# Kernel optimization log

Measured on AMD Instinct MI355X. Metric: run time of the kernel, lower is better.

The kernel has to match this reference:

```python
import jax, jax.numpy as jnp
import numpy as np

ENC_HID = 512
DEC_HID = 1024
ATTN_DIM = 1024
ATTN_IN = ENC_HID * 2 + DEC_HID  # 2048
B, S = 32, 1024


def setup_inputs() -> dict:
    key = jax.random.key(0)
    k1, k2, k3, k4, k5 = jax.random.split(key, 5)
    decoder_hidden = jax.random.normal(k1, (B, DEC_HID), dtype=jnp.float32)
    encoder_outputs = jax.random.normal(k2, (B, S, 2 * ENC_HID), dtype=jnp.float32)
    # nn.Linear(attn_in, attn_dim): weight [attn_dim, attn_in], bias [attn_dim]
    lim = 1.0 / np.sqrt(ATTN_IN)
    W = jax.random.uniform(k3, (ATTN_IN, ATTN_DIM), jnp.float32, -lim, lim)
    b = jax.random.uniform(k4, (ATTN_DIM,), jnp.float32, -lim, lim)
    v = jax.random.uniform(k5, (ATTN_DIM,), jnp.float32, 0.0, 1.0)
    return {"decoder_hidden": decoder_hidden, "encoder_outputs": encoder_outputs,
            "W": W, "b": b, "v": v}


def reference(decoder_hidden, encoder_outputs, W, b, v):
    # Avoid materializing the repeat+concat: split the Linear weight into the
    # decoder-hidden block and the encoder-outputs block. Same math as
    # tanh(Linear(cat([dec_rep, enc], -1))).
    W_dec = W[:DEC_HID]          # [dec_hid, attn_dim]
    W_enc = W[DEC_HID:]          # [2*enc_hid, attn_dim]
    dec_proj = decoder_hidden @ W_dec + b                     # [B, A]
    enc_proj = jnp.einsum('bse,ea->bsa', encoder_outputs, W_enc)  # [B, S, A]
    energy = jnp.tanh(enc_proj + dec_proj[:, None, :])        # [B, S, A]
    attention = jnp.einsum('bsa,a->bs', energy, v)            # [B, S]
    return jax.nn.softmax(attention, axis=1)
```

## Files before the change

### kernel.cpp

```cpp
#include <hip/hip_runtime.h>
#include <stdint.h>

#define ENC2 1024
#define DECH 1024
#define ADIM 1024
#define BB   32
#define SS   1024

typedef _Float16 half_t;
typedef __attribute__((ext_vector_type(8))) _Float16 half8;
typedef __attribute__((ext_vector_type(4))) float    f32x4;

__device__ __forceinline__ void dma16(const half_t* g, half_t* l) {
    __builtin_amdgcn_global_load_lds((const __attribute__((address_space(1))) void*)g,
                                     (__attribute__((address_space(3))) void*)l,
                                     16, 0, 0);
}

__global__ __launch_bounds__(256) void k_wt(const float* __restrict__ W,
                                            half_t* __restrict__ Wt2) {
    __shared__ float tile[32][257];
    const int nb = blockIdx.x >> 5;
    const int ks = blockIdx.x & 31;
    const int t = threadIdx.x;
    #pragma unroll
    for (int i = 0; i < 32; i++) {
        int idx = t + i * 256;
        int kr = idx >> 8, n = idx & 255;
        tile[kr][n] = W[(size_t)(DECH + ks * 32 + kr) * ADIM + nb * 256 + n];
    }
    __syncthreads();
    half_t* reg = Wt2 + ((size_t)(nb * 32 + ks) << 13);
    #pragma unroll
    for (int i = 0; i < 4; i++) {
        int cid = t + i * 256;
        int r = cid >> 2, pos = cid & 3;
        int c = pos ^ ((r >> 1) & 3);
        half8 h;
        #pragma unroll
        for (int e = 0; e < 8; e++) h[e] = (half_t)tile[c * 8 + e][r];
        *(half8*)(reg + r * 32 + pos * 8) = h;
    }
}

__global__ __launch_bounds__(256) void k_dp1(const float* __restrict__ dh,
                                             const float* __restrict__ W,
                                             float* __restrict__ part) {
    __shared__ float red[4][BB][64];
    const int t = threadIdx.x;
    const int ct = blockIdx.x & 15;
    const int kc = blockIdx.x >> 4;
    const int col = ct * 64 + (t & 63);
    const int w = t >> 6;
    const int k0 = kc * 128 + w * 32;
    float wreg[32];
    #pragma unroll
    for (int kk = 0; kk < 32; kk++)
        wreg[kk] = W[(size_t)(k0 + kk) * ADIM + col];
    float s[BB];
    #pragma unroll
    for (int b = 0; b < BB; b++) s[b] = 0.f;
    #pragma unroll
    for (int kk = 0; kk < 32; kk++) {
        #pragma unroll
        for (int b = 0; b < BB; b++)
            s[b] += dh[b * DECH + k0 + kk] * wreg[kk];
    }
    #pragma unroll
    for (int b = 0; b < BB; b++) red[w][b][t & 63] = s[b];
    __syncthreads();
    if (t < 64) {
        for (int b = 0; b < BB; b++)
            part[((size_t)kc * BB + b) * ADIM + ct * 64 + t] =
                red[0][b][t] + red[1][b][t] + red[2][b][t] + red[3][b][t];
    }
}

__global__ __launch_bounds__(256) void k_dp2(const float* __restrict__ part,
                                             const float* __restrict__ bias,
                                             float* __restrict__ decp) {
    const int i = blockIdx.x * 256 + threadIdx.x;
    float s = bias[i & (ADIM - 1)];
    #pragma unroll
    for (int kc = 0; kc < 8; kc++)
        s += part[(size_t)kc * BB * ADIM + i];
    decp[i] = s;
}

#define BM 128
#define BN 256
#define BK 32
#define LDA 40

__global__ __launch_bounds__(512, 4) void k_main(const float* __restrict__ enc,
                                                 const half_t* __restrict__ Wt2,
                                                 const float* __restrict__ decp,
                                                 const float* __restrict__ v,
                                                 float* __restrict__ scores_part) {
    __shared__ half_t lsA[2][BM][LDA];
    __shared__ half_t lsB[2][BN * BK];

    const int bid = blockIdx.x;
    const int mi = (bid >> 5) * 8 + (bid & 7);
    const int nb = (bid >> 3) & 3;
    const int m0 = mi * BM;
    const int t = threadIdx.x;
    const int w = t >> 6, L = t & 63;
    const int wm = w & 1, wn = w >> 1;
    const int lane15 = L & 15, quad = L >> 4;

    const int arow = t & 127;
    const int akc  = (t >> 7) * 8;
    const float* Aptr = enc + (size_t)(m0 + arow) * ENC2 + akc;

    const half_t* Bbase = Wt2 + ((size_t)(nb * 32) << 13);

    f32x4 acc[4][4];
    #pragma unroll
    for (int i = 0; i < 4; i++)
        #pragma unroll
        for (int j = 0; j < 4; j++) acc[i][j] = (f32x4)0.f;

    float4 ra0, ra1;
    auto loadA = [&](int ks) {
        const float* p = Aptr + ks * BK;
        ra0 = *(const float4*)p;
        ra1 = *(const float4*)(p + 4);
    };
    auto writeA = [&](int pb) {
        half8 ha;
        ha[0] = (half_t)ra0.x; ha[1] = (half_t)ra0.y;
        ha[2] = (half_t)ra0.z; ha[3] = (half_t)ra0.w;
        ha[4] = (half_t)ra1.x; ha[5] = (half_t)ra1.y;
        ha[6] = (half_t)ra1.z; ha[7] = (half_t)ra1.w;
        *(half8*)&lsA[pb][arow][akc] = ha;
    };
    auto dmaB = [&](int ks, int pb) {
        #pragma unroll
        for (int jj = 0; jj < 2; jj++) {
            int j = 2 * w + jj;
            dma16(Bbase + ((size_t)ks << 13) + j * 512 + L * 8,
                  &lsB[pb][j * 512]);
        }
    };

    dmaB(0, 0);
    loadA(0);
    writeA(0);
    loadA(1);
    __syncthreads();

    for (int ks = 0; ks < ENC2 / BK; ks++) {
        const int cur = ks & 1;
        if (ks < ENC2 / BK - 1) {
            dmaB(ks + 1, cur ^ 1);
            writeA(cur ^ 1);
            if (ks < ENC2 / BK - 2) loadA(ks + 2);
        }
        half8 af[4], bf[4];
        #pragma unroll
        for (int sm = 0; sm < 4; sm++)
            af[sm] = *(const half8*)&lsA[cur][wm * 64 + sm * 16 + lane15][quad * 8];
        #pragma unroll
        for (int sn = 0; sn < 4; sn++) {
            int r = wn * 64 + sn * 16 + lane15;
            int pos = quad ^ ((r >> 1) & 3);
            bf[sn] = *(const half8*)&lsB[cur][r * 32 + pos * 8];
        }
        #pragma unroll
        for (int sm = 0; sm < 4; sm++)
            #pragma unroll
            for (int sn = 0; sn < 4; sn++)
                acc[sm][sn] = __builtin_amdgcn_mfma_f32_16x16x32_f16(
                    af[sm], bf[sn], acc[sm][sn], 0, 0, 0);
        __syncthreads();
    }

    const int batch = mi >> 3;
    float vv[4], dp[4];
    #pragma unroll
    for (int sn = 0; sn < 4; sn++) {
        int ng = nb * BN + wn * 64 + sn * 16 + lane15;
        vv[sn] = v[ng];
        dp[sn] = decp[(size_t)batch * ADIM + ng];
    }

    float* redL = (float*)&lsA[0][0][0];
    #pragma unroll
    for (int sm = 0; sm < 4; sm++) {
        #pragma unroll
        for (int rr = 0; rr < 4; rr++) {
            float s = 0.f;
            #pragma unroll
            for (int sn = 0; sn < 4; sn++) {
                float x = acc[sm][sn][rr] + dp[sn];
                float e  = __builtin_amdgcn_exp2f(x * 2.8853900817779268f);
                float th = 1.f - 2.f * __builtin_amdgcn_rcpf(e + 1.f);
                s += th * vv[sn];
            }
            s += __shfl_xor(s, 1, 64);
            s += __shfl_xor(s, 2, 64);
            s += __shfl_xor(s, 4, 64);
            s += __shfl_xor(s, 8, 64);
            if (lane15 == 0) {
                int mlocal = wm * 64 + sm * 16 + quad * 4 + rr;
                redL[wn * 128 + mlocal] = s;
            }
        }
    }
    __syncthreads();
    if (t < 128) {
        float s = redL[t] + redL[128 + t] + redL[256 + t] + redL[384 + t];
        scores_part[((size_t)nb << 15) + m0 + t] = s;
    }
}

__global__ __launch_bounds__(256) void k_softmax(const float* __restrict__ sp,
                                                 float* __restrict__ out) {
    __shared__ float red[8];
    const int b = blockIdx.x, t = threadIdx.x;
    float x[4];
    #pragma unroll
    for (int i = 0; i < 4; i++) {
        size_t idx = (size_t)b * SS + t + i * 256;
        x[i] = sp[idx] + sp[(1u << 15) + idx] + sp[(2u << 15) + idx] +
               sp[(3u << 15) + idx];
    }
    float mx = fmaxf(fmaxf(x[0], x[1]), fmaxf(x[2], x[3]));
    #pragma unroll
    for (int d = 1; d < 64; d <<= 1) mx = fmaxf(mx, __shfl_xor(mx, d, 64));
    if ((t & 63) == 0) red[t >> 6] = mx;
    __syncthreads();
    mx = fmaxf(fmaxf(red[0], red[1]), fmaxf(red[2], red[3]));
    float e[4], s = 0.f;
    #pragma unroll
    for (int i = 0; i < 4; i++) {
        e[i] = __builtin_amdgcn_exp2f((x[i] - mx) * 1.4426950408889634f);
        s += e[i];
    }
    #pragma unroll
    for (int d = 1; d < 64; d <<= 1) s += __shfl_xor(s, d, 64);
    if ((t & 63) == 0) red[4 + (t >> 6)] = s;
    __syncthreads();
    s = red[4] + red[5] + red[6] + red[7];
    float inv = 1.f / s;
    #pragma unroll
    for (int i = 0; i < 4; i++) out[(size_t)b * SS + t + i * 256] = e[i] * inv;
}

extern "C" void kernel_launch(void* const* d_in, const int* in_sizes, int n_in,
                              void* d_out, int out_size, void* d_ws, size_t ws_size,
                              hipStream_t stream) {
    const float* dh   = (const float*)d_in[0];
    const float* enc  = (const float*)d_in[1];
    const float* W    = (const float*)d_in[2];
    const float* bias = (const float*)d_in[3];
    const float* v    = (const float*)d_in[4];
    float* out = (float*)d_out;

    char* ws = (char*)d_ws;
    half_t* Wt2   = (half_t*)ws;
    float*  decp  = (float*)(ws + 2u * 1024 * 1024);
    float*  spart = (float*)(ws + 2u * 1024 * 1024 + 128 * 1024);
    float*  dpart = (float*)(ws + 2u * 1024 * 1024 + 640 * 1024);

    k_wt     <<<128, 256, 0, stream>>>(W, Wt2);
    k_dp1    <<<128, 256, 0, stream>>>(dh, W, dpart);
    k_dp2    <<<128, 256, 0, stream>>>(dpart, bias, decp);
    k_main   <<<1024, 512, 0, stream>>>(enc, Wt2, decp, v, spart);
    k_softmax<<<32, 256, 0, stream>>>(spart, out);
}
```

Before: 308.1 us.

## Pre-convert encoder outputs to fp16 tiles and DMA them directly into LDS

Adds a prep pass that converts the fp32 encoder outputs to fp16 in a layout that matches the MFMA tiles. The same launch also fuses the weight transpose and the decoder-projection partial kernels into one grid. The main GEMM then loads A with global_load_lds DMA instead of register loads plus conversion, and folds the dp2 reduction into its epilogue. The cost is an extra 64MB fp16 round trip through the workspace, plus a fallback path that keeps the old code when the workspace is too small.

```diff
diff --git a/kernel.cpp b/kernel.cpp
--- a/kernel.cpp
+++ b/kernel.cpp
@@ -8,6 +8,7 @@
 #define SS   1024
 
 typedef _Float16 half_t;
+typedef __attribute__((ext_vector_type(4))) _Float16 half4;
 typedef __attribute__((ext_vector_type(8))) _Float16 half8;
 typedef __attribute__((ext_vector_type(4))) float    f32x4;
 
@@ -17,12 +18,13 @@
                                      16, 0, 0);
 }
 
-__global__ __launch_bounds__(256) void k_wt(const float* __restrict__ W,
-                                            half_t* __restrict__ Wt2) {
-    __shared__ float tile[32][257];
-    const int nb = blockIdx.x >> 5;
-    const int ks = blockIdx.x & 31;
-    const int t = threadIdx.x;
+
+__device__ __forceinline__ void wt_body(int blk, int t, char* smem,
+                                        const float* __restrict__ W,
+                                        half_t* __restrict__ Wt2) {
+    float (*tile)[257] = (float (*)[257])smem;
+    const int nb = blk >> 5;
+    const int ks = blk & 31;
     #pragma unroll
     for (int i = 0; i < 32; i++) {
         int idx = t + i * 256;
@@ -43,13 +45,13 @@
     }
 }
 
-__global__ __launch_bounds__(256) void k_dp1(const float* __restrict__ dh,
-                                             const float* __restrict__ W,
-                                             float* __restrict__ part) {
-    __shared__ float red[4][BB][64];
-    const int t = threadIdx.x;
-    const int ct = blockIdx.x & 15;
-    const int kc = blockIdx.x >> 4;
+__device__ __forceinline__ void dp1_body(int blk, int t, char* smem,
+                                         const float* __restrict__ dh,
+                                         const float* __restrict__ W,
+                                         float* __restrict__ part) {
+    float (*red)[BB][64] = (float (*)[BB][64])smem;
+    const int ct = blk & 15;
+    const int kc = blk >> 4;
     const int col = ct * 64 + (t & 63);
     const int w = t >> 6;
     const int k0 = kc * 128 + w * 32;
@@ -76,15 +78,47 @@
     }
 }
 
-__global__ __launch_bounds__(256) void k_dp2(const float* __restrict__ part,
-                                             const float* __restrict__ bias,
-                                             float* __restrict__ decp) {
-    const int i = blockIdx.x * 256 + threadIdx.x;
-    float s = bias[i & (ADIM - 1)];
-    #pragma unroll
-    for (int kc = 0; kc < 8; kc++)
-        s += part[(size_t)kc * BB * ADIM + i];
-    decp[i] = s;
+__device__ __forceinline__ void enc16_body(int blk, int t, char* smem,
+                                           const float* __restrict__ enc,
+                                           half_t* __restrict__ e16) {
+    half_t (*Lt)[264] = (half_t (*)[264])smem;
+    const int rblk = blk >> 2, cblk = blk & 3;
+    const int r0 = rblk * 64, k0 = cblk * 256;
+    #pragma unroll
+    for (int i = 0; i < 16; i++) {
+        int row = i * 4 + (t >> 6);
+        int col = (t & 63) * 4;
+        float4 vv = *(const float4*)&enc[(size_t)(r0 + row) * ENC2 + k0 + col];
+        half4 h;
+        h[0] = (half_t)vv.x; h[1] = (half_t)vv.y;
+        h[2] = (half_t)vv.z; h[3] = (half_t)vv.w;
+        *(half4*)&Lt[row][col] = h;
+    }
+    __syncthreads();
+    const int mi = rblk >> 1, p = rblk & 1;
+    const int ks0 = cblk * 8;
+    #pragma unroll
+    for (int j = 0; j < 8; j++) {
+        int u = j * 256 + t;
+        int pair = u >> 6, l = u & 63;
+        int ksl = pair >> 2, quad = pair & 3;
+        half8 h = *(const half8*)&Lt[l][ksl * 32 + quad * 8];
+        size_t chunk = (size_t)(mi * 32 + ks0 + ksl) * 8 + quad * 2 + p;
+        *(half8*)&e16[(chunk << 9) + l * 8] = h;
+    }
+}
+
+__global__ __launch_bounds__(256) void k_prep(const float* __restrict__ enc,
+                                              const float* __restrict__ W,
+                                              const float* __restrict__ dh,
+                                              half_t* __restrict__ e16,
+                                              half_t* __restrict__ Wt2,
+                                              float* __restrict__ dpart) {
+    __shared__ __align__(16) char smem[33792];
+    const int bid = blockIdx.x;
+    if (bid < 2048)       enc16_body(bid, threadIdx.x, smem, enc, e16);
+    else if (bid < 2176)  wt_body(bid - 2048, threadIdx.x, smem, W, Wt2);
+    else                  dp1_body(bid - 2176, threadIdx.x, smem, dh, W, dpart);
 }
 
 #define BM 128
@@ -92,13 +126,14 @@
 #define BK 32
 #define LDA 40
 
-__global__ __launch_bounds__(512, 4) void k_main(const float* __restrict__ enc,
+__global__ __launch_bounds__(512, 4) void k_main(const half_t* __restrict__ encA,
                                                  const half_t* __restrict__ Wt2,
-                                                 const float* __restrict__ decp,
+                                                 const float* __restrict__ dpart,
+                                                 const float* __restrict__ bias,
                                                  const float* __restrict__ v,
                                                  float* __restrict__ scores_part) {
-    __shared__ half_t lsA[2][BM][LDA];
-    __shared__ half_t lsB[2][BN * BK];
+    __shared__ half_t lsA[2][4096];
+    __shared__ half_t lsB[2][8192];
 
     const int bid = blockIdx.x;
     const int mi = (bid >> 5) * 8 + (bid & 7);
@@ -109,10 +144,7 @@
     const int wm = w & 1, wn = w >> 1;
     const int lane15 = L & 15, quad = L >> 4;
 
-    const int arow = t & 127;
-    const int akc  = (t >> 7) * 8;
-    const float* Aptr = enc + (size_t)(m0 + arow) * ENC2 + akc;
-
+    const half_t* Abase = encA + ((size_t)mi << 17);
     const half_t* Bbase = Wt2 + ((size_t)(nb * 32) << 13);
 
     f32x4 acc[4][4];
@@ -121,19 +153,8 @@
         #pragma unroll
         for (int j = 0; j < 4; j++) acc[i][j] = (f32x4)0.f;
 
-    float4 ra0, ra1;
-    auto loadA = [&](int ks) {
-        const float* p = Aptr + ks * BK;
-        ra0 = *(const float4*)p;
-        ra1 = *(const float4*)(p + 4);
-    };
-    auto writeA = [&](int pb) {
-        half8 ha;
-        ha[0] = (half_t)ra0.x; ha[1] = (half_t)ra0.y;
-        ha[2] = (half_t)ra0.z; ha[3] = (half_t)ra0.w;
-        ha[4] = (half_t)ra1.x; ha[5] = (half_t)ra1.y;
-        ha[6] = (half_t)ra1.z; ha[7] = (half_t)ra1.w;
-        *(half8*)&lsA[pb][arow][akc] = ha;
+    auto dmaA = [&](int ks, int pb) {
+        dma16(Abase + (((size_t)ks * 8 + w) << 9) + L * 8, &lsA[pb][w * 512]);
     };
     auto dmaB = [&](int ks, int pb) {
         #pragma unroll
@@ -144,23 +165,21 @@
         }
     };
 
+    dmaA(0, 0);
     dmaB(0, 0);
-    loadA(0);
-    writeA(0);
-    loadA(1);
     __syncthreads();
 
     for (int ks = 0; ks < ENC2 / BK; ks++) {
         const int cur = ks & 1;
         if (ks < ENC2 / BK - 1) {
+            dmaA(ks + 1, cur ^ 1);
             dmaB(ks + 1, cur ^ 1);
-            writeA(cur ^ 1);
-            if (ks < ENC2 / BK - 2) loadA(ks + 2);
         }
         half8 af[4], bf[4];
         #pragma unroll
         for (int sm = 0; sm < 4; sm++)
-            af[sm] = *(const half8*)&lsA[cur][wm * 64 + sm * 16 + lane15][quad * 8];
+            af[sm] = *(const half8*)&lsA[cur][quad * 1024 +
+                                              (wm * 64 + sm * 16 + lane15) * 8];
         #pragma unroll
         for (int sn = 0; sn < 4; sn++) {
             int r = wn * 64 + sn * 16 + lane15;
@@ -182,10 +201,14 @@
     for (int sn = 0; sn < 4; sn++) {
         int ng = nb * BN + wn * 64 + sn * 16 + lane15;
         vv[sn] = v[ng];
-        dp[sn] = decp[(size_t)batch * ADIM + ng];
-    }
-
-    float* redL = (float*)&lsA[0][0][0];
+        float s = bias[ng];
+        #pragma unroll
+        for (int kc = 0; kc < 8; kc++)
+            s += dpart[((size_t)kc * BB + batch) * ADIM + ng];
+        dp[sn] = s;
+    }
+
+    float* redL = (float*)&lsA[0][0];
     #pragma unroll
     for (int sm = 0; sm < 4; sm++) {
         #pragma unroll
@@ -248,6 +271,152 @@
     for (int i = 0; i < 4; i++) out[(size_t)b * SS + t + i * 256] = e[i] * inv;
 }
 
+__global__ __launch_bounds__(256) void k_wt_f(const float* __restrict__ W,
+                                              half_t* __restrict__ Wt2) {
+    __shared__ __align__(16) char smem[32896];
+    wt_body(blockIdx.x, threadIdx.x, smem, W, Wt2);
+}
+
+__global__ __launch_bounds__(256) void k_dp1_f(const float* __restrict__ dh,
+                                               const float* __restrict__ W,
+                                               float* __restrict__ part) {
+    __shared__ __align__(16) char smem[32768];
+    dp1_body(blockIdx.x, threadIdx.x, smem, dh, W, part);
+}
+
+__global__ __launch_bounds__(256) void k_dp2_f(const float* __restrict__ part,
+                                               const float* __restrict__ bias,
+                                               float* __restrict__ decp) {
+    const int i = blockIdx.x * 256 + threadIdx.x;
+    float s = bias[i & (ADIM - 1)];
+    #pragma unroll
+    for (int kc = 0; kc < 8; kc++)
+        s += part[(size_t)kc * BB * ADIM + i];
+    decp[i] = s;
+}
+
+__global__ __launch_bounds__(512, 4) void k_main_reg(const float* __restrict__ enc,
+                                                     const half_t* __restrict__ Wt2,
+                                                     const float* __restrict__ decp,
+                                                     const float* __restrict__ v,
+                                                     float* __restrict__ scores_part) {
+    __shared__ half_t lsA[2][BM][LDA];
+    __shared__ half_t lsB[2][BN * BK];
+
+    const int bid = blockIdx.x;
+    const int mi = (bid >> 5) * 8 + (bid & 7);
+    const int nb = (bid >> 3) & 3;
+    const int m0 = mi * BM;
+    const int t = threadIdx.x;
+    const int w = t >> 6, L = t & 63;
+    const int wm = w & 1, wn = w >> 1;
+    const int lane15 = L & 15, quad = L >> 4;
+
+    const int arow = t & 127;
+    const int akc  = (t >> 7) * 8;
+    const float* Aptr = enc + (size_t)(m0 + arow) * ENC2 + akc;
+    const half_t* Bbase = Wt2 + ((size_t)(nb * 32) << 13);
+
+    f32x4 acc[4][4];
+    #pragma unroll
+    for (int i = 0; i < 4; i++)
+        #pragma unroll
+        for (int j = 0; j < 4; j++) acc[i][j] = (f32x4)0.f;
+
+    float4 ra0, ra1;
+    auto loadA = [&](int ks) {
+        const float* p = Aptr + ks * BK;
+        ra0 = *(const float4*)p;
+        ra1 = *(const float4*)(p + 4);
+    };
+    auto writeA = [&](int pb) {
+        half8 ha;
+        ha[0] = (half_t)ra0.x; ha[1] = (half_t)ra0.y;
+        ha[2] = (half_t)ra0.z; ha[3] = (half_t)ra0.w;
+        ha[4] = (half_t)ra1.x; ha[5] = (half_t)ra1.y;
+        ha[6] = (half_t)ra1.z; ha[7] = (half_t)ra1.w;
+        *(half8*)&lsA[pb][arow][akc] = ha;
+    };
+    auto dmaB = [&](int ks, int pb) {
+        #pragma unroll
+        for (int jj = 0; jj < 2; jj++) {
+            int j = 2 * w + jj;
+            dma16(Bbase + ((size_t)ks << 13) + j * 512 + L * 8,
+                  &lsB[pb][j * 512]);
+        }
+    };
+
+    dmaB(0, 0);
+    loadA(0);
+    writeA(0);
+    loadA(1);
+    __syncthreads();
+
+    for (int ks = 0; ks < ENC2 / BK; ks++) {
+        const int cur = ks & 1;
+        if (ks < ENC2 / BK - 1) {
+            dmaB(ks + 1, cur ^ 1);
+            writeA(cur ^ 1);
+            if (ks < ENC2 / BK - 2) loadA(ks + 2);
+        }
+        half8 af[4], bf[4];
+        #pragma unroll
+        for (int sm = 0; sm < 4; sm++)
+            af[sm] = *(const half8*)&lsA[cur][wm * 64 + sm * 16 + lane15][quad * 8];
+        #pragma unroll
+        for (int sn = 0; sn < 4; sn++) {
+            int r = wn * 64 + sn * 16 + lane15;
+            int pos = quad ^ ((r >> 1) & 3);
+            bf[sn] = *(const half8*)&lsB[cur][r * 32 + pos * 8];
+        }
+        #pragma unroll
+        for (int sm = 0; sm < 4; sm++)
+            #pragma unroll
+            for (int sn = 0; sn < 4; sn++)
+                acc[sm][sn] = __builtin_amdgcn_mfma_f32_16x16x32_f16(
+                    af[sm], bf[sn], acc[sm][sn], 0, 0, 0);
+        __syncthreads();
+    }
+
+    const int batch = mi >> 3;
+    float vv[4], dp[4];
+    #pragma unroll
+    for (int sn = 0; sn < 4; sn++) {
+        int ng = nb * BN + wn * 64 + sn * 16 + lane15;
+        vv[sn] = v[ng];
+        dp[sn] = decp[(size_t)batch * ADIM + ng];
+    }
+
+    float* redL = (float*)&lsA[0][0][0];
+    #pragma unroll
+    for (int sm = 0; sm < 4; sm++) {
+        #pragma unroll
+        for (int rr = 0; rr < 4; rr++) {
+            float s = 0.f;
+            #pragma unroll
+            for (int sn = 0; sn < 4; sn++) {
+                float x = acc[sm][sn][rr] + dp[sn];
+                float e  = __builtin_amdgcn_exp2f(x * 2.8853900817779268f);
+                float th = 1.f - 2.f * __builtin_amdgcn_rcpf(e + 1.f);
+                s += th * vv[sn];
+            }
+            s += __shfl_xor(s, 1, 64);
+            s += __shfl_xor(s, 2, 64);
+            s += __shfl_xor(s, 4, 64);
+            s += __shfl_xor(s, 8, 64);
+            if (lane15 == 0) {
+                int mlocal = wm * 64 + sm * 16 + quad * 4 + rr;
+                redL[wn * 128 + mlocal] = s;
+            }
+        }
+    }
+    __syncthreads();
+    if (t < 128) {
+        float s = redL[t] + redL[128 + t] + redL[256 + t] + redL[384 + t];
+        scores_part[((size_t)nb << 15) + m0 + t] = s;
+    }
+}
+
 extern "C" void kernel_launch(void* const* d_in, const int* in_sizes, int n_in,
                               void* d_out, int out_size, void* d_ws, size_t ws_size,
                               hipStream_t stream) {
@@ -259,14 +428,28 @@
     float* out = (float*)d_out;
 
     char* ws = (char*)d_ws;
-    half_t* Wt2   = (half_t*)ws;
-    float*  decp  = (float*)(ws + 2u * 1024 * 1024);
-    float*  spart = (float*)(ws + 2u * 1024 * 1024 + 128 * 1024);
-    float*  dpart = (float*)(ws + 2u * 1024 * 1024 + 640 * 1024);
-
-    k_wt     <<<128, 256, 0, stream>>>(W, Wt2);
-    k_dp1    <<<128, 256, 0, stream>>>(dh, W, dpart);
-    k_dp2    <<<128, 256, 0, stream>>>(dpart, bias, decp);
-    k_main   <<<1024, 512, 0, stream>>>(enc, Wt2, decp, v, spart);
-    k_softmax<<<32, 256, 0, stream>>>(spart, out);
-}
+    const size_t E16_BYTES = (size_t)BB * SS * ENC2 * sizeof(half_t);
+    const size_t NEED = (4u << 20) + E16_BYTES;
+
+    if (ws_size >= NEED) {
+        half_t* Wt2   = (half_t*)ws;
+        float*  dpart = (float*)(ws + (2u << 20));
+        float*  spart = (float*)(ws + (3u << 20));
+        half_t* e16   = (half_t*)(ws + (4u << 20));
+
+        k_prep   <<<2304, 256, 0, stream>>>(enc, W, dh, e16, Wt2, dpart);
+        k_main   <<<1024, 512, 0, stream>>>(e16, Wt2, dpart, bias, v, spart);
+        k_softmax<<<32, 256, 0, stream>>>(spart, out);
+    } else {
+        half_t* Wt2   = (half_t*)ws;
+        float*  decp  = (float*)(ws + 2u * 1024 * 1024);
+        float*  spart = (float*)(ws + 2u * 1024 * 1024 + 128 * 1024);
+        float*  dpart = (float*)(ws + 2u * 1024 * 1024 + 640 * 1024);
+
+        k_wt_f   <<<128, 256, 0, stream>>>(W, Wt2);
+        k_dp1_f  <<<128, 256, 0, stream>>>(dh, W, dpart);
+        k_dp2_f  <<<128, 256, 0, stream>>>(dpart, bias, decp);
+        k_main_reg<<<1024, 512, 0, stream>>>(enc, Wt2, decp, v, spart);
+        k_softmax<<<32, 256, 0, stream>>>(spart, out);
+    }
+}
```

Result: faster. 294.1 us (-4.5%).
